# Kernel tuning notes

Hardware: AMD Instinct MI355X
Metric: run time of the kernel (lower is better)

Reference implementation:

```python
import jax, jax.numpy as jnp
import numpy as np
from jax import lax

VOCAB, EMB, H, L_CTX = 5, 64, 256, 100
HG = 2 * H  # generator hidden = 512


def lstm_cell(x, h, c, Wih, Whh, b):
    # PyTorch gate order: i, f, g, o
    z = x @ Wih.T + h @ Whh.T + b
    i, f, g, o = jnp.split(z, 4, axis=-1)
    c = jax.nn.sigmoid(f) * c + jax.nn.sigmoid(i) * jnp.tanh(g)
    h = jax.nn.sigmoid(o) * jnp.tanh(c)
    return h, c


def run_lstm(xs, Wih, Whh, b, hidden):
    # xs: [T, B, D] -> ys: [T, B, hidden]
    B = xs.shape[1]
    h0 = jnp.zeros((B, hidden), xs.dtype)

    def step(carry, x):
        h, c = carry
        h, c = lstm_cell(x, h, c, Wih, Whh, b)
        return (h, c), h

    _, ys = lax.scan(step, (h0, h0), xs)
    return ys


def bidir_layer(xs, Wih, Whh, b):
    # Wih/Whh/b stacked over directions: [2, ...]
    yf = run_lstm(xs, Wih[0], Whh[0], b[0], H)
    yb = run_lstm(xs[::-1], Wih[1], Whh[1], b[1], H)[::-1]
    return jnp.concatenate([yf, yb], axis=-1)  # [T, B, 2H]


def setup_inputs() -> dict:
    key = jax.random.key(0)
    ks = iter(jax.random.split(key, 24))
    s = 1.0 / np.sqrt(H)  # pytorch-style uniform scale -> use normal*s

    def w(shape):
        return (jax.random.normal(next(ks), shape, jnp.float32) * s).astype(jnp.float32)

    B = 1024
    inp = {
        "left_context": jax.random.randint(next(ks), (B, L_CTX), 0, VOCAB),
        "right_context": jax.random.randint(next(ks), (B, L_CTX), 0, VOCAB),
        "target_length": 256,
        "emb": w((VOCAB, EMB)),
        # bidirectional context LSTM, layer 0 (in=64) and layer 1 (in=512)
        "ctx0_Wih": w((2, 4 * H, EMB)),
        "ctx0_Whh": w((2, 4 * H, H)),
        "ctx0_b": w((2, 4 * H)),
        "ctx1_Wih": w((2, 4 * H, 2 * H)),
        "ctx1_Whh": w((2, 4 * H, H)),
        "ctx1_b": w((2, 4 * H)),
        # generator LSTM (hidden=512), layer 0 (in=64) and layer 1 (in=512)
        "gen0_Wih": w((4 * HG, EMB)),
        "gen0_Whh": w((4 * HG, HG)),
        "gen0_b": w((4 * HG,)),
        "gen1_Wih": w((4 * HG, HG)),
        "gen1_Whh": w((4 * HG, HG)),
        "gen1_b": w((4 * HG,)),
        "out_W": w((VOCAB, HG)),
        "out_b": w((VOCAB,)),
    }
    return inp


def reference(left_context, right_context, target_length, emb,
              ctx0_Wih, ctx0_Whh, ctx0_b, ctx1_Wih, ctx1_Whh, ctx1_b,
              gen0_Wih, gen0_Whh, gen0_b, gen1_Wih, gen1_Whh, gen1_b,
              out_W, out_b):
    B = left_context.shape[0]

    def encode(tokens):
        x = emb[tokens].transpose(1, 0, 2)          # [L, B, 64]
        x = bidir_layer(x, ctx0_Wih, ctx0_Whh, ctx0_b)  # dropout: eval -> identity
        x = bidir_layer(x, ctx1_Wih, ctx1_Whh, ctx1_b)
        return x                                     # [L, B, 512]

    left_final = encode(left_context)[-1]            # [B, 512]
    right_final = encode(right_context)[0]           # [B, 512]
    combined = (left_final + right_final) * 0.5

    # h_0 = combined repeated over both generator layers; c_0 = 0
    zeros = jnp.zeros((B, HG), combined.dtype)
    tok0 = jnp.zeros((B,), jnp.int32)

    def dec_step(carry, _):
        h0, c0, h1, c1, tok = carry
        x = emb[tok]                                 # [B, 64]
        h0, c0 = lstm_cell(x, h0, c0, gen0_Wih, gen0_Whh, gen0_b)
        h1, c1 = lstm_cell(h0, h1, c1, gen1_Wih, gen1_Whh, gen1_b)
        logits = h1 @ out_W.T + out_b                # dropout: eval -> identity
        tok = jnp.argmax(logits, axis=-1)
        return (h0, c0, h1, c1, tok), logits

    _, logits = lax.scan(dec_step, (combined, zeros, combined, zeros, tok0),
                         None, length=target_length)
    return logits.transpose(1, 0, 2)                 # [B, T, vocab]
```

## Files before the change

### kernel.cpp

```cpp
#include <hip/hip_runtime.h>


#define L_SEQ 100
#define BATCH 1024
#define HCTX 256
#define HG 512
#define TDEC 256

typedef __attribute__((ext_vector_type(8))) short bf16x8;
typedef __attribute__((ext_vector_type(4))) float f32x4;

__device__ __forceinline__ float sigf(float x){ return 1.0f/(1.0f+expf(-x)); }
__device__ __forceinline__ unsigned short f2bf(float x){
  unsigned int u = __float_as_uint(x);
  return (unsigned short)((u + 0x7fffu + ((u>>16)&1u)) >> 16);
}
__device__ __forceinline__ float bf2f(unsigned short h){
  return __uint_as_float(((unsigned int)h)<<16);
}

__global__ void pack_w(const float* __restrict__ W, int G, int K, int KTtot, int kt0,
                       unsigned short* __restrict__ hi, unsigned short* __restrict__ lo){
  int idx = blockIdx.x*blockDim.x + threadIdx.x;
  int kt_n = K/32;
  int total = (G/16)*kt_n*64;
  if (idx >= total) return;
  int lane = idx & 63;
  int ktl = (idx>>6) % kt_n;
  int gt  = (idx>>6) / kt_n;
  int g = gt*16 + (lane & 15);
  int k = ktl*32 + (lane>>4)*8;
  const float* src = W + (size_t)g*K + k;
  size_t dst = (((size_t)gt*KTtot + (kt0 + ktl))*64 + lane)*8;
  #pragma unroll
  for (int j=0;j<8;j++){
    float x = src[j];
    unsigned short h = f2bf(x);
    hi[dst+j] = h;
    lo[dst+j] = f2bf(x - bf2f(h));
  }
}

__global__ void embprep(const float* __restrict__ emb,
                        const float* __restrict__ c0Wih, const float* __restrict__ c0b,
                        const float* __restrict__ g0Wih, const float* __restrict__ g0b,
                        float* __restrict__ ectx0, float* __restrict__ egen0){
  int idx = blockIdx.x*blockDim.x + threadIdx.x;
  if (idx < 2*5*1024){
    int d = idx / 5120;
    int v = (idx / 1024) % 5;
    int j = idx % 1024;
    const float* w = c0Wih + ((size_t)d*1024 + j)*64;
    const float* e = emb + v*64;
    float s = c0b[d*1024 + j];
    #pragma unroll
    for (int k=0;k<64;k++) s += e[k]*w[k];
    ectx0[idx] = s;
  } else if (idx < 2*5*1024 + 5*2048){
    int i2 = idx - 10240;
    int v = i2 / 2048;
    int j = i2 % 2048;
    const float* w = g0Wih + (size_t)j*64;
    const float* e = emb + v*64;
    float s = g0b[j];
    #pragma unroll
    for (int k=0;k<64;k++) s += e[k]*w[k];
    egen0[i2] = s;
  }
}

__global__ void __launch_bounds__(512,1) ctx_l0_mfma(
    const int* __restrict__ toks,
    const float* __restrict__ ectx0,
    const unsigned short* __restrict__ wh, const unsigned short* __restrict__ wl,
    unsigned short* __restrict__ y0h, unsigned short* __restrict__ y0l)
{
  const int id  = blockIdx.x;
  const int dir = (id >> 2) & 1;
  const int bx  = ((id >> 3) << 2) | (id & 3);
  const int e0  = bx * 16;
  const int lane = threadIdx.x & 63;
  const int w    = threadIdx.x >> 6;
  const int lo16 = lane & 15, kgrp = lane >> 4;

  __shared__ unsigned short hsh[16*256];
  __shared__ unsigned short hsl[16*256];
  __shared__ float cs[16*256];
  for (int i=threadIdx.x;i<16*256;i+=512){ hsh[i]=0; hsl[i]=0; cs[i]=0.f; }
  __syncthreads();

  const unsigned short* pbh[4][2];
  const unsigned short* pbl[4][2];
  #pragma unroll
  for (int g=0;g<4;g++){
    #pragma unroll
    for (int st=0;st<2;st++){
      int ct = g*16 + w*2 + st;
      size_t off = (size_t)dir*1024*256 + ((size_t)(ct*8)*64 + lane)*8;
      pbh[g][st] = wh + off; pbl[g][st] = wl + off;
    }
  }
  const unsigned aoff0 = (unsigned)(lo16*512 + kgrp*16);
  const unsigned axor  = ((unsigned)(lo16 & 7)) << 4;

  for (int s=0;s<L_SEQ;s++){
    const int t = dir ? (L_SEQ-1-s) : s;
    f32x4 zero = {0.f,0.f,0.f,0.f};
    f32x4 acc[4][2];
    #pragma unroll
    for (int g=0;g<4;g++){
      #pragma unroll
      for (int st=0;st<2;st++) acc[g][st] = zero;
    }
    #pragma unroll 2
    for (int kt=0;kt<8;kt++){
      unsigned ao = (aoff0 + kt*64) ^ axor;
      bf16x8 ah = *(const bf16x8*)((const char*)hsh + ao);
      bf16x8 al = *(const bf16x8*)((const char*)hsl + ao);
      #pragma unroll
      for (int g=0;g<4;g++){
        #pragma unroll
        for (int st=0;st<2;st++){
          bf16x8 bh = *(const bf16x8*)(pbh[g][st] + (size_t)kt*512);
          bf16x8 bl = *(const bf16x8*)(pbl[g][st] + (size_t)kt*512);
          acc[g][st] = __builtin_amdgcn_mfma_f32_16x16x32_bf16(ah,bh,acc[g][st],0,0,0);
          acc[g][st] = __builtin_amdgcn_mfma_f32_16x16x32_bf16(al,bh,acc[g][st],0,0,0);
          acc[g][st] = __builtin_amdgcn_mfma_f32_16x16x32_bf16(ah,bl,acc[g][st],0,0,0);
        }
      }
    }
    __syncthreads();
    int tkr[4];
    #pragma unroll
    for (int r=0;r<4;r++) tkr[r] = toks[(e0 + kgrp*4 + r)*L_SEQ + t];
    #pragma unroll
    for (int st=0;st<2;st++){
      const int unit = w*32 + st*16 + lo16;
      #pragma unroll
      for (int r=0;r<4;r++){
        const int row = kgrp*4 + r;
        const int e = e0 + row;
        const float* ep = ectx0 + ((size_t)(dir*5 + tkr[r]))*1024 + unit;
        float zi = acc[0][st][r] + ep[0];
        float zf = acc[1][st][r] + ep[256];
        float zg = acc[2][st][r] + ep[512];
        float zo = acc[3][st][r] + ep[768];
        int ci = row*256 + unit;
        float c = sigf(zf)*cs[ci] + sigf(zi)*tanhf(zg);
        float h = sigf(zo)*tanhf(c);
        cs[ci] = c;
        unsigned short hb = f2bf(h), lb = f2bf(h - bf2f(hb));
        unsigned hoff = ((unsigned)(row*512 + unit*2)) ^ (((unsigned)(row & 7)) << 4);
        *(unsigned short*)((char*)hsh + hoff) = hb;
        *(unsigned short*)((char*)hsl + hoff) = lb;
        size_t yo = ((size_t)t*BATCH + e)*512 + dir*256 + unit;
        y0h[yo] = hb; y0l[yo] = lb;
      }
    }
    __syncthreads();
  }
}

__global__ void __launch_bounds__(512,1) ctx_l1_mfma(
    const unsigned short* __restrict__ y0h, const unsigned short* __restrict__ y0l,
    const unsigned short* __restrict__ wh, const unsigned short* __restrict__ wl,
    const float* __restrict__ bias,
    float* __restrict__ finals, int t_store)
{
  const int id  = blockIdx.x;
  const int dir = (id >> 2) & 1;
  const int bx  = ((id >> 3) << 2) | (id & 3);
  const int e0  = bx * 16;
  const int lane = threadIdx.x & 63;
  const int w    = threadIdx.x >> 6;
  const int lo16 = lane & 15, kgrp = lane >> 4;

  __shared__ unsigned short xsh[16*512];
  __shared__ unsigned short xsl[16*512];
  __shared__ unsigned short hsh[16*256];
  __shared__ unsigned short hsl[16*256];
  __shared__ float cs[16*256];
  for (int i=threadIdx.x;i<16*256;i+=512){ hsh[i]=0; hsl[i]=0; cs[i]=0.f; }

  float bb[4][2];
  #pragma unroll
  for (int g=0;g<4;g++){
    #pragma unroll
    for (int st=0;st<2;st++)
      bb[g][st] = bias[dir*1024 + g*256 + w*32 + st*16 + lo16];
  }
  const unsigned short* pbh[4][2];
  const unsigned short* pbl[4][2];
  #pragma unroll
  for (int g=0;g<4;g++){
    #pragma unroll
    for (int st=0;st<2;st++){
      int ct = g*16 + w*2 + st;
      size_t off = (size_t)dir*1024*768 + ((size_t)(ct*24)*64 + lane)*8;
      pbh[g][st] = wh + off; pbl[g][st] = wl + off;
    }
  }
  const unsigned axor = ((unsigned)(lo16 & 7)) << 4;
  __syncthreads();

  for (int s=0;s<L_SEQ;s++){
    const int t = dir ? (L_SEQ-1-s) : s;
    #pragma unroll
    for (int cc=0; cc<2; cc++){
      int ci = threadIdx.x + cc*512;
      int row = ci >> 6, cr = ci & 63;
      const unsigned short* srcbase = y0h + ((size_t)t*BATCH + e0 + row)*512 + cr*8;
      const unsigned short* srcbasel = y0l + ((size_t)t*BATCH + e0 + row)*512 + cr*8;
      uint4 vh = *(const uint4*)srcbase;
      uint4 vl = *(const uint4*)srcbasel;
      unsigned xo = ((unsigned)(row*1024 + cr*16)) ^ (((unsigned)(row & 7)) << 4);
      *(uint4*)((char*)xsh + xo) = vh;
      *(uint4*)((char*)xsl + xo) = vl;
    }
    __syncthreads();
    f32x4 zero = {0.f,0.f,0.f,0.f};
    f32x4 acc[4][2];
    #pragma unroll
    for (int g=0;g<4;g++){
      #pragma unroll
      for (int st=0;st<2;st++) acc[g][st] = zero;
    }
    #pragma unroll 2
    for (int kt=0;kt<16;kt++){
      unsigned ao = ((unsigned)(lo16*1024 + kt*64 + kgrp*16)) ^ axor;
      bf16x8 ah = *(const bf16x8*)((const char*)xsh + ao);
      bf16x8 al = *(const bf16x8*)((const char*)xsl + ao);
      #pragma unroll
      for (int g=0;g<4;g++){
        #pragma unroll
        for (int st=0;st<2;st++){
          bf16x8 bh = *(const bf16x8*)(pbh[g][st] + (size_t)kt*512);
          bf16x8 bl = *(const bf16x8*)(pbl[g][st] + (size_t)kt*512);
          acc[g][st] = __builtin_amdgcn_mfma_f32_16x16x32_bf16(ah,bh,acc[g][st],0,0,0);
          acc[g][st] = __builtin_amdgcn_mfma_f32_16x16x32_bf16(al,bh,acc[g][st],0,0,0);
          acc[g][st] = __builtin_amdgcn_mfma_f32_16x16x32_bf16(ah,bl,acc[g][st],0,0,0);
        }
      }
    }
    #pragma unroll 2
    for (int kt=16;kt<24;kt++){
      unsigned ao = ((unsigned)(lo16*512 + (kt-16)*64 + kgrp*16)) ^ axor;
      bf16x8 ah = *(const bf16x8*)((const char*)hsh + ao);
      bf16x8 al = *(const bf16x8*)((const char*)hsl + ao);
      #pragma unroll
      for (int g=0;g<4;g++){
        #pragma unroll
        for (int st=0;st<2;st++){
          bf16x8 bh = *(const bf16x8*)(pbh[g][st] + (size_t)kt*512);
          bf16x8 bl = *(const bf16x8*)(pbl[g][st] + (size_t)kt*512);
          acc[g][st] = __builtin_amdgcn_mfma_f32_16x16x32_bf16(ah,bh,acc[g][st],0,0,0);
          acc[g][st] = __builtin_amdgcn_mfma_f32_16x16x32_bf16(al,bh,acc[g][st],0,0,0);
          acc[g][st] = __builtin_amdgcn_mfma_f32_16x16x32_bf16(ah,bl,acc[g][st],0,0,0);
        }
      }
    }
    __syncthreads();
    #pragma unroll
    for (int st=0;st<2;st++){
      const int unit = w*32 + st*16 + lo16;
      #pragma unroll
      for (int r=0;r<4;r++){
        const int row = kgrp*4 + r;
        float zi = acc[0][st][r] + bb[0][st];
        float zf = acc[1][st][r] + bb[1][st];
        float zg = acc[2][st][r] + bb[2][st];
        float zo = acc[3][st][r] + bb[3][st];
        int ci = row*256 + unit;
        float c = sigf(zf)*cs[ci] + sigf(zi)*tanhf(zg);
        float h = sigf(zo)*tanhf(c);
        cs[ci] = c;
        unsigned short hb = f2bf(h), lb = f2bf(h - bf2f(hb));
        unsigned hoff = ((unsigned)(row*512 + unit*2)) ^ (((unsigned)(row & 7)) << 4);
        *(unsigned short*)((char*)hsh + hoff) = hb;
        *(unsigned short*)((char*)hsl + hoff) = lb;
        if (t == t_store)
          finals[(size_t)(e0 + row)*512 + dir*256 + unit] = h;
      }
    }
    __syncthreads();
  }
}

__global__ void combine_init2(const float* __restrict__ lf, const float* __restrict__ rf,
                              unsigned short* __restrict__ h0h, unsigned short* __restrict__ h0l,
                              unsigned short* __restrict__ h1h, unsigned short* __restrict__ h1l,
                              float* __restrict__ c0, float* __restrict__ c1){
  int i = blockIdx.x*blockDim.x + threadIdx.x;
  if (i < BATCH*HG){
    float v = 0.5f*(lf[i]+rf[i]);
    unsigned short h = f2bf(v);
    unsigned short l = f2bf(v - bf2f(h));
    h0h[i]=h; h0l[i]=l; h1h[i]=h; h1l[i]=l;
    c0[i]=0.f; c1[i]=0.f;
  }
}

__global__ void __launch_bounds__(512,1) dec_l0_mfma(
    const float* __restrict__ egen0,
    const unsigned short* __restrict__ wh, const unsigned short* __restrict__ wl,
    const unsigned short* __restrict__ hih, const unsigned short* __restrict__ hil,
    const unsigned short* __restrict__ h1ih, const unsigned short* __restrict__ h1il,
    unsigned short* __restrict__ hoh, unsigned short* __restrict__ hol,
    float* __restrict__ cst,
    const float* __restrict__ outW, const float* __restrict__ outb,
    float* __restrict__ out, int t)
{
  __shared__ unsigned short bsm[2][32768];
  const int bid = blockIdx.x;
  const int by = bid & 15;
  const int bx = bid >> 4;
  const int e0 = bx * 64;
  const int lane = threadIdx.x & 63;
  const int w = threadIdx.x >> 6;
  const int wm = w & 3, wu = w >> 2;
  const int ut = by*2 + wu;
  const int lo16 = lane & 15, kgrp = lane >> 4;
  const int arow = e0 + wm*16 + lo16;
  const int u = ut*16 + lo16;
  const int r0 = e0 + wm*16 + kgrp*4;

  const unsigned short* pah = hih + (size_t)arow*512 + kgrp*8;
  const unsigned short* pal = hil + (size_t)arow*512 + kgrp*8;

  auto STAGE = [&](int c){
    #pragma unroll
    for (int i=0;i<8;i++){
      int id = w*8 + i;
      int hl  = id & 1;
      int q   = (id >> 1) & 3;
      int wu2 = (id >> 3) & 1;
      int ksl = id >> 4;
      int ks  = c*4 + ksl;
      const unsigned short* src = (hl ? wl : wh)
          + (((size_t)(q*32 + by*2 + wu2)*16 + ks)*64 + lane)*8;
      __builtin_amdgcn_global_load_lds((const void*)src,
          (void*)(&bsm[c & 1][id*512]), 16, 0, 0);
    }
  };

  const f32x4 z4 = {0.f,0.f,0.f,0.f};
  f32x4 aHH[4]={z4,z4,z4,z4}, aLH[4]={z4,z4,z4,z4}, aHL[4]={z4,z4,z4,z4};

  STAGE(0);
  __syncthreads();
  for (int c=0; c<4; c++){
    if (c+1 < 4) STAGE(c+1);
    const unsigned short* bb = &bsm[c&1][0];
    #pragma unroll
    for (int ksl=0; ksl<4; ksl++){
      int ks = c*4 + ksl;
      bf16x8 ah = *(const bf16x8*)(pah + (size_t)ks*32);
      bf16x8 al = *(const bf16x8*)(pal + (size_t)ks*32);
      #pragma unroll
      for (int q=0;q<4;q++){
        int fid = ((ksl*2 + wu)*4 + q)*2;
        bf16x8 bh = *(const bf16x8*)(bb + fid*512     + lane*8);
        bf16x8 bl = *(const bf16x8*)(bb + fid*512+512 + lane*8);
        aHH[q] = __builtin_amdgcn_mfma_f32_16x16x32_bf16(ah, bh, aHH[q], 0,0,0);
        aLH[q] = __builtin_amdgcn_mfma_f32_16x16x32_bf16(al, bh, aLH[q], 0,0,0);
        aHL[q] = __builtin_amdgcn_mfma_f32_16x16x32_bf16(ah, bl, aHL[q], 0,0,0);
      }
    }
    __syncthreads();
  }

  int tkr[4] = {0,0,0,0};
  if (t > 0){
    float acc5[4][5];
    #pragma unroll
    for (int r=0;r<4;r++){
      #pragma unroll
      for (int v=0;v<5;v++) acc5[r][v]=0.f;
    }
    #pragma unroll
    for (int j=0;j<4;j++){
      const int ub = lo16*32 + j*8;
      f32x4 w0[5], w1[5];
      #pragma unroll
      for (int v=0;v<5;v++){
        const float* wp = outW + v*512 + ub;
        w0[v] = *(const f32x4*)(wp);
        w1[v] = *(const f32x4*)(wp+4);
      }
      #pragma unroll
      for (int r=0;r<4;r++){
        const unsigned short* hh = h1ih + (size_t)(r0+r)*512 + ub;
        const unsigned short* hl = h1il + (size_t)(r0+r)*512 + ub;
        bf16x8 vh = *(const bf16x8*)hh;
        bf16x8 vl = *(const bf16x8*)hl;
        #pragma unroll
        for (int m=0;m<4;m++){
          float hv = bf2f((unsigned short)vh[m]) + bf2f((unsigned short)vl[m]);
          #pragma unroll
          for (int v=0;v<5;v++) acc5[r][v] += hv * w0[v][m];
        }
        #pragma unroll
        for (int m=0;m<4;m++){
          float hv = bf2f((unsigned short)vh[m+4]) + bf2f((unsigned short)vl[m+4]);
          #pragma unroll
          for (int v=0;v<5;v++) acc5[r][v] += hv * w1[v][m];
        }
      }
    }
    #pragma unroll
    for (int r=0;r<4;r++){
      #pragma unroll
      for (int v=0;v<5;v++){
        float s = acc5[r][v];
        s += __shfl_xor(s, 1);
        s += __shfl_xor(s, 2);
        s += __shfl_xor(s, 4);
        s += __shfl_xor(s, 8);
        acc5[r][v] = s + outb[v];
      }
      float best = acc5[r][0]; int tk = 0;
      if (acc5[r][1] > best){ best = acc5[r][1]; tk = 1; }
      if (acc5[r][2] > best){ best = acc5[r][2]; tk = 2; }
      if (acc5[r][3] > best){ best = acc5[r][3]; tk = 3; }
      if (acc5[r][4] > best){ best = acc5[r][4]; tk = 4; }
      tkr[r] = tk;
    }
    if (by == 0 && wu == 0 && lo16 == 0){
      #pragma unroll
      for (int r=0;r<4;r++){
        float* op = out + ((size_t)(r0+r)*TDEC + (t-1))*5;
        #pragma unroll
        for (int v=0;v<5;v++) op[v] = acc5[r][v];
      }
    }
  }

  #pragma unroll
  for (int r=0;r<4;r++){
    const int e = r0 + r;
    const float* ep = egen0 + (size_t)tkr[r]*2048 + u;
    float zi = aHH[0][r]+aLH[0][r]+aHL[0][r] + ep[0];
    float zf = aHH[1][r]+aLH[1][r]+aHL[1][r] + ep[512];
    float zg = aHH[2][r]+aLH[2][r]+aHL[2][r] + ep[1024];
    float zo = aHH[3][r]+aLH[3][r]+aHL[3][r] + ep[1536];
    const size_t idx = (size_t)e*512 + u;
    float c = sigf(zf)*cst[idx] + sigf(zi)*tanhf(zg);
    float h = sigf(zo)*tanhf(c);
    cst[idx] = c;
    unsigned short hb = f2bf(h);
    hoh[idx] = hb;
    hol[idx] = f2bf(h - bf2f(hb));
  }
}

__global__ void __launch_bounds__(512,1) dec_l1_mfma(
    const unsigned short* __restrict__ xh, const unsigned short* __restrict__ xl,
    const unsigned short* __restrict__ wh, const unsigned short* __restrict__ wl,
    const float* __restrict__ bias,
    const unsigned short* __restrict__ hih, const unsigned short* __restrict__ hil,
    unsigned short* __restrict__ hoh, unsigned short* __restrict__ hol,
    float* __restrict__ cst)
{
  __shared__ unsigned short bsm[2][32768];
  const int bid = blockIdx.x;
  const int by = bid & 15;
  const int bx = bid >> 4;
  const int e0 = bx * 64;
  const int lane = threadIdx.x & 63;
  const int w = threadIdx.x >> 6;
  const int wm = w & 3, wu = w >> 2;
  const int ut = by*2 + wu;
  const int lo16 = lane & 15, kgrp = lane >> 4;
  const int arow = e0 + wm*16 + lo16;
  const int u = ut*16 + lo16;
  const int r0 = e0 + wm*16 + kgrp*4;

  const unsigned short* pxh = xh  + (size_t)arow*512 + kgrp*8;
  const unsigned short* pxl = xl  + (size_t)arow*512 + kgrp*8;
  const unsigned short* pah = hih + (size_t)arow*512 + kgrp*8;
  const unsigned short* pal = hil + (size_t)arow*512 + kgrp*8;

  auto STAGE = [&](int c){
    #pragma unroll
    for (int i=0;i<8;i++){
      int id = w*8 + i;
      int hl  = id & 1;
      int q   = (id >> 1) & 3;
      int wu2 = (id >> 3) & 1;
      int ksl = id >> 4;
      int ks  = c*4 + ksl;
      const unsigned short* src = (hl ? wl : wh)
          + (((size_t)(q*32 + by*2 + wu2)*32 + ks)*64 + lane)*8;
      __builtin_amdgcn_global_load_lds((const void*)src,
          (void*)(&bsm[c & 1][id*512]), 16, 0, 0);
    }
  };

  const f32x4 z4 = {0.f,0.f,0.f,0.f};
  f32x4 aHH[4]={z4,z4,z4,z4}, aLH[4]={z4,z4,z4,z4}, aHL[4]={z4,z4,z4,z4};

  STAGE(0);
  __syncthreads();
  for (int c=0; c<8; c++){
    if (c+1 < 8) STAGE(c+1);
    const unsigned short* bb = &bsm[c&1][0];
    const unsigned short* pAh = (c < 4) ? pxh : pah;
    const unsigned short* pAl = (c < 4) ? pxl : pal;
    const int ksA = (c & 3)*4;
    #pragma unroll
    for (int ksl=0; ksl<4; ksl++){
      bf16x8 ah = *(const bf16x8*)(pAh + (size_t)(ksA+ksl)*32);
      bf16x8 al = *(const bf16x8*)(pAl + (size_t)(ksA+ksl)*32);
      #pragma unroll
      for (int q=0;q<4;q++){
        int fid = ((ksl*2 + wu)*4 + q)*2;
        bf16x8 bh = *(const bf16x8*)(bb + fid*512     + lane*8);
        bf16x8 bl = *(const bf16x8*)(bb + fid*512+512 + lane*8);
        aHH[q] = __builtin_amdgcn_mfma_f32_16x16x32_bf16(ah, bh, aHH[q], 0,0,0);
        aLH[q] = __builtin_amdgcn_mfma_f32_16x16x32_bf16(al, bh, aLH[q], 0,0,0);
        aHL[q] = __builtin_amdgcn_mfma_f32_16x16x32_bf16(ah, bl, aHL[q], 0,0,0);
      }
    }
    __syncthreads();
  }

  const float b0 = bias[u], b1 = bias[512+u], b2 = bias[1024+u], b3 = bias[1536+u];
  #pragma unroll
  for (int r=0;r<4;r++){
    const int e = r0 + r;
    float zi = aHH[0][r]+aLH[0][r]+aHL[0][r] + b0;
    float zf = aHH[1][r]+aLH[1][r]+aHL[1][r] + b1;
    float zg = aHH[2][r]+aLH[2][r]+aHL[2][r] + b2;
    float zo = aHH[3][r]+aLH[3][r]+aHL[3][r] + b3;
    const size_t idx = (size_t)e*512 + u;
    float c = sigf(zf)*cst[idx] + sigf(zi)*tanhf(zg);
    float h = sigf(zo)*tanhf(c);
    cst[idx] = c;
    unsigned short hb = f2bf(h);
    hoh[idx] = hb;
    hol[idx] = f2bf(h - bf2f(hb));
  }
}

__global__ void dec_outF(const unsigned short* __restrict__ h1h,
                         const unsigned short* __restrict__ h1l,
                         const float* __restrict__ outW,
                         const float* __restrict__ outb,
                         float* __restrict__ out){
  const int lane = threadIdx.x & 63;
  const int e = blockIdx.x*4 + (threadIdx.x >> 6);
  const unsigned short* hh = h1h + (size_t)e*512;
  const unsigned short* hl = h1l + (size_t)e*512;
  float s0=0,s1=0,s2=0,s3=0,s4=0;
  for (int k=lane;k<512;k+=64){
    float hv = bf2f(hh[k]) + bf2f(hl[k]);
    s0 += hv*outW[k];
    s1 += hv*outW[512+k];
    s2 += hv*outW[1024+k];
    s3 += hv*outW[1536+k];
    s4 += hv*outW[2048+k];
  }
  #pragma unroll
  for (int off=32; off>0; off>>=1){
    s0 += __shfl_down(s0, off);
    s1 += __shfl_down(s1, off);
    s2 += __shfl_down(s2, off);
    s3 += __shfl_down(s3, off);
    s4 += __shfl_down(s4, off);
  }
  if (lane==0){
    float* op = out + ((size_t)e*TDEC + (TDEC-1))*5;
    op[0]=s0+outb[0]; op[1]=s1+outb[1]; op[2]=s2+outb[2];
    op[3]=s3+outb[3]; op[4]=s4+outb[4];
  }
}

extern "C" void kernel_launch(void* const* d_in, const int* in_sizes, int n_in,
                              void* d_out, int out_size, void* d_ws, size_t ws_size,
                              hipStream_t stream){
  (void)in_sizes; (void)n_in; (void)out_size;
  const int*   leftc    = (const int*)d_in[0];
  const int*   rightc   = (const int*)d_in[1];
  const float* emb      = (const float*)d_in[3];
  const float* ctx0_Wih = (const float*)d_in[4];
  const float* ctx0_Whh = (const float*)d_in[5];
  const float* ctx0_b   = (const float*)d_in[6];
  const float* ctx1_Wih = (const float*)d_in[7];
  const float* ctx1_Whh = (const float*)d_in[8];
  const float* ctx1_b   = (const float*)d_in[9];
  const float* gen0_Wih = (const float*)d_in[10];
  const float* gen0_Whh = (const float*)d_in[11];
  const float* gen0_b   = (const float*)d_in[12];
  const float* gen1_Wih = (const float*)d_in[13];
  const float* gen1_Whh = (const float*)d_in[14];
  const float* gen1_b   = (const float*)d_in[15];
  const float* out_W    = (const float*)d_in[16];
  const float* out_b    = (const float*)d_in[17];
  float* out = (float*)d_out;

  char* p = (char*)d_ws;
  auto carve = [&](size_t nfloats)->float*{
    float* r = (float*)p;
    p += ((nfloats*sizeof(float) + 255) & ~(size_t)255);
    return r;
  };
  auto carveu = [&](size_t nush)->unsigned short*{
    return (unsigned short*)carve((nush + 1)/2);
  };
  float* ectx0  = carve(2*5*1024);
  float* egen0  = carve(5*2048);
  float* leftF  = carve((size_t)BATCH*HG);
  float* rightF = carve((size_t)BATCH*HG);
  float* c0s    = carve((size_t)BATCH*HG);
  float* c1s    = carve((size_t)BATCH*HG);
  unsigned short* c0pkh = carveu((size_t)2*1024*256);
  unsigned short* c0pkl = carveu((size_t)2*1024*256);
  unsigned short* c1pkh = carveu((size_t)2*1024*768);
  unsigned short* c1pkl = carveu((size_t)2*1024*768);
  unsigned short* pk0h = carveu((size_t)2048*512);
  unsigned short* pk0l = carveu((size_t)2048*512);
  unsigned short* pk1h = carveu((size_t)2048*1024);
  unsigned short* pk1l = carveu((size_t)2048*1024);
  unsigned short* h0ha = carveu((size_t)BATCH*HG);
  unsigned short* h0la = carveu((size_t)BATCH*HG);
  unsigned short* h0hb = carveu((size_t)BATCH*HG);
  unsigned short* h0lb = carveu((size_t)BATCH*HG);
  unsigned short* h1ha = carveu((size_t)BATCH*HG);
  unsigned short* h1la = carveu((size_t)BATCH*HG);
  unsigned short* h1hb = carveu((size_t)BATCH*HG);
  unsigned short* h1lb = carveu((size_t)BATCH*HG);
  unsigned short* y0h = carveu((size_t)L_SEQ*BATCH*512);
  unsigned short* y0l = carveu((size_t)L_SEQ*BATCH*512);
  if ((size_t)(p - (char*)d_ws) > ws_size) return;

  for (int d=0; d<2; d++){
    pack_w<<<128, 256, 0, stream>>>(ctx0_Whh + (size_t)d*1024*256, 1024, 256, 8, 0,
                                    c0pkh + (size_t)d*262144, c0pkl + (size_t)d*262144);
    pack_w<<<256, 256, 0, stream>>>(ctx1_Wih + (size_t)d*1024*512, 1024, 512, 24, 0,
                                    c1pkh + (size_t)d*786432, c1pkl + (size_t)d*786432);
    pack_w<<<128, 256, 0, stream>>>(ctx1_Whh + (size_t)d*1024*256, 1024, 256, 24, 16,
                                    c1pkh + (size_t)d*786432, c1pkl + (size_t)d*786432);
  }
  pack_w<<<512, 256, 0, stream>>>(gen0_Whh, 2048, 512, 16,  0, pk0h, pk0l);
  pack_w<<<512, 256, 0, stream>>>(gen1_Wih, 2048, 512, 32,  0, pk1h, pk1l);
  pack_w<<<512, 256, 0, stream>>>(gen1_Whh, 2048, 512, 32, 16, pk1h, pk1l);

  embprep<<<(20480+255)/256, 256, 0, stream>>>(emb, ctx0_Wih, ctx0_b,
                                               gen0_Wih, gen0_b, ectx0, egen0);

  ctx_l0_mfma<<<128, 512, 0, stream>>>(leftc, ectx0, c0pkh, c0pkl, y0h, y0l);
  ctx_l1_mfma<<<128, 512, 0, stream>>>(y0h, y0l, c1pkh, c1pkl, ctx1_b, leftF, L_SEQ-1);
  ctx_l0_mfma<<<128, 512, 0, stream>>>(rightc, ectx0, c0pkh, c0pkl, y0h, y0l);
  ctx_l1_mfma<<<128, 512, 0, stream>>>(y0h, y0l, c1pkh, c1pkl, ctx1_b, rightF, 0);

  combine_init2<<<(BATCH*HG+255)/256, 256, 0, stream>>>(leftF, rightF,
                                                        h0ha, h0la, h1ha, h1la,
                                                        c0s, c1s);

  for (int t=0;t<TDEC;t++){
    unsigned short* h0ih = (t&1)? h0hb : h0ha;
    unsigned short* h0il = (t&1)? h0lb : h0la;
    unsigned short* h0oh = (t&1)? h0ha : h0hb;
    unsigned short* h0ol = (t&1)? h0la : h0lb;
    unsigned short* h1ih = (t&1)? h1hb : h1ha;
    unsigned short* h1il = (t&1)? h1lb : h1la;
    unsigned short* h1oh = (t&1)? h1ha : h1hb;
    unsigned short* h1ol = (t&1)? h1la : h1lb;
    dec_l0_mfma<<<256, 512, 0, stream>>>(egen0, pk0h, pk0l,
                                         h0ih, h0il, h1ih, h1il,
                                         h0oh, h0ol, c0s,
                                         out_W, out_b, out, t);
    dec_l1_mfma<<<256, 512, 0, stream>>>(h0oh, h0ol, pk1h, pk1l, gen1_b,
                                         h1ih, h1il, h1oh, h1ol, c1s);
  }
  dec_outF<<<256, 256, 0, stream>>>(h1ha, h1la, out_W, out_b, out);
}
```

Baseline: 22.96 ms.

## Fuse decoder time loop into one persistent cooperative kernel with grid sync

Replaces the 512 per-step decoder kernel launches with a single cooperative kernel that loops over all 256 timesteps and uses grid.sync between layers. LSTM cell states now stay in registers instead of global memory, and the first weight stage of the next layer is prefetched across phase boundaries. This is meant to remove launch overhead and cell-state traffic. The cost is two grid-wide barriers per step, and it requires all 256 blocks to be co-resident.

After: 44.38 ms. 93.3% more time.

```diff
diff --git a/kernel.cpp b/kernel.cpp
--- a/kernel.cpp
+++ b/kernel.cpp
@@ -1,4 +1,7 @@
 #include <hip/hip_runtime.h>
+#include <hip/hip_cooperative_groups.h>
+
+namespace cg = cooperative_groups;
 
 
 #define L_SEQ 100
@@ -288,28 +291,29 @@
 
 __global__ void combine_init2(const float* __restrict__ lf, const float* __restrict__ rf,
                               unsigned short* __restrict__ h0h, unsigned short* __restrict__ h0l,
-                              unsigned short* __restrict__ h1h, unsigned short* __restrict__ h1l,
-                              float* __restrict__ c0, float* __restrict__ c1){
+                              unsigned short* __restrict__ h1h, unsigned short* __restrict__ h1l){
   int i = blockIdx.x*blockDim.x + threadIdx.x;
   if (i < BATCH*HG){
     float v = 0.5f*(lf[i]+rf[i]);
     unsigned short h = f2bf(v);
     unsigned short l = f2bf(v - bf2f(h));
     h0h[i]=h; h0l[i]=l; h1h[i]=h; h1l[i]=l;
-    c0[i]=0.f; c1[i]=0.f;
-  }
-}
-
-__global__ void __launch_bounds__(512,1) dec_l0_mfma(
+  }
+}
+
+__global__ void __launch_bounds__(512,1) dec_persist(
     const float* __restrict__ egen0,
-    const unsigned short* __restrict__ wh, const unsigned short* __restrict__ wl,
-    const unsigned short* __restrict__ hih, const unsigned short* __restrict__ hil,
-    const unsigned short* __restrict__ h1ih, const unsigned short* __restrict__ h1il,
-    unsigned short* __restrict__ hoh, unsigned short* __restrict__ hol,
-    float* __restrict__ cst,
+    const unsigned short* __restrict__ w0h, const unsigned short* __restrict__ w0l,
+    const unsigned short* __restrict__ w1h, const unsigned short* __restrict__ w1l,
+    const float* __restrict__ bias1,
     const float* __restrict__ outW, const float* __restrict__ outb,
-    float* __restrict__ out, int t)
+    unsigned short* __restrict__ h0ha, unsigned short* __restrict__ h0la,
+    unsigned short* __restrict__ h0hb, unsigned short* __restrict__ h0lb,
+    unsigned short* __restrict__ h1ha, unsigned short* __restrict__ h1la,
+    unsigned short* __restrict__ h1hb, unsigned short* __restrict__ h1lb,
+    float* __restrict__ out)
 {
+  cg::grid_group grid = cg::this_grid();
   __shared__ unsigned short bsm[2][32768];
   const int bid = blockIdx.x;
   const int by = bid & 15;
@@ -324,10 +328,10 @@
   const int u = ut*16 + lo16;
   const int r0 = e0 + wm*16 + kgrp*4;
 
-  const unsigned short* pah = hih + (size_t)arow*512 + kgrp*8;
-  const unsigned short* pal = hil + (size_t)arow*512 + kgrp*8;
-
-  auto STAGE = [&](int c){
+  const float b10 = bias1[u], b11 = bias1[512+u];
+  const float b12 = bias1[1024+u], b13 = bias1[1536+u];
+
+  auto STAGE0 = [&](int c){
     #pragma unroll
     for (int i=0;i<8;i++){
       int id = w*8 + i;
@@ -336,151 +340,13 @@
       int wu2 = (id >> 3) & 1;
       int ksl = id >> 4;
       int ks  = c*4 + ksl;
-      const unsigned short* src = (hl ? wl : wh)
+      const unsigned short* src = (hl ? w0l : w0h)
           + (((size_t)(q*32 + by*2 + wu2)*16 + ks)*64 + lane)*8;
       __builtin_amdgcn_global_load_lds((const void*)src,
           (void*)(&bsm[c & 1][id*512]), 16, 0, 0);
     }
   };
-
-  const f32x4 z4 = {0.f,0.f,0.f,0.f};
-  f32x4 aHH[4]={z4,z4,z4,z4}, aLH[4]={z4,z4,z4,z4}, aHL[4]={z4,z4,z4,z4};
-
-  STAGE(0);
-  __syncthreads();
-  for (int c=0; c<4; c++){
-    if (c+1 < 4) STAGE(c+1);
-    const unsigned short* bb = &bsm[c&1][0];
-    #pragma unroll
-    for (int ksl=0; ksl<4; ksl++){
-      int ks = c*4 + ksl;
-      bf16x8 ah = *(const bf16x8*)(pah + (size_t)ks*32);
-      bf16x8 al = *(const bf16x8*)(pal + (size_t)ks*32);
-      #pragma unroll
-      for (int q=0;q<4;q++){
-        int fid = ((ksl*2 + wu)*4 + q)*2;
-        bf16x8 bh = *(const bf16x8*)(bb + fid*512     + lane*8);
-        bf16x8 bl = *(const bf16x8*)(bb + fid*512+512 + lane*8);
-        aHH[q] = __builtin_amdgcn_mfma_f32_16x16x32_bf16(ah, bh, aHH[q], 0,0,0);
-        aLH[q] = __builtin_amdgcn_mfma_f32_16x16x32_bf16(al, bh, aLH[q], 0,0,0);
-        aHL[q] = __builtin_amdgcn_mfma_f32_16x16x32_bf16(ah, bl, aHL[q], 0,0,0);
-      }
-    }
-    __syncthreads();
-  }
-
-  int tkr[4] = {0,0,0,0};
-  if (t > 0){
-    float acc5[4][5];
-    #pragma unroll
-    for (int r=0;r<4;r++){
-      #pragma unroll
-      for (int v=0;v<5;v++) acc5[r][v]=0.f;
-    }
-    #pragma unroll
-    for (int j=0;j<4;j++){
-      const int ub = lo16*32 + j*8;
-      f32x4 w0[5], w1[5];
-      #pragma unroll
-      for (int v=0;v<5;v++){
-        const float* wp = outW + v*512 + ub;
-        w0[v] = *(const f32x4*)(wp);
-        w1[v] = *(const f32x4*)(wp+4);
-      }
-      #pragma unroll
-      for (int r=0;r<4;r++){
-        const unsigned short* hh = h1ih + (size_t)(r0+r)*512 + ub;
-        const unsigned short* hl = h1il + (size_t)(r0+r)*512 + ub;
-        bf16x8 vh = *(const bf16x8*)hh;
-        bf16x8 vl = *(const bf16x8*)hl;
-        #pragma unroll
-        for (int m=0;m<4;m++){
-          float hv = bf2f((unsigned short)vh[m]) + bf2f((unsigned short)vl[m]);
-          #pragma unroll
-          for (int v=0;v<5;v++) acc5[r][v] += hv * w0[v][m];
-        }
-        #pragma unroll
-        for (int m=0;m<4;m++){
-          float hv = bf2f((unsigned short)vh[m+4]) + bf2f((unsigned short)vl[m+4]);
-          #pragma unroll
-          for (int v=0;v<5;v++) acc5[r][v] += hv * w1[v][m];
-        }
-      }
-    }
-    #pragma unroll
-    for (int r=0;r<4;r++){
-      #pragma unroll
-      for (int v=0;v<5;v++){
-        float s = acc5[r][v];
-        s += __shfl_xor(s, 1);
-        s += __shfl_xor(s, 2);
-        s += __shfl_xor(s, 4);
-        s += __shfl_xor(s, 8);
-        acc5[r][v] = s + outb[v];
-      }
-      float best = acc5[r][0]; int tk = 0;
-      if (acc5[r][1] > best){ best = acc5[r][1]; tk = 1; }
-      if (acc5[r][2] > best){ best = acc5[r][2]; tk = 2; }
-      if (acc5[r][3] > best){ best = acc5[r][3]; tk = 3; }
-      if (acc5[r][4] > best){ best = acc5[r][4]; tk = 4; }
-      tkr[r] = tk;
-    }
-    if (by == 0 && wu == 0 && lo16 == 0){
-      #pragma unroll
-      for (int r=0;r<4;r++){
-        float* op = out + ((size_t)(r0+r)*TDEC + (t-1))*5;
-        #pragma unroll
-        for (int v=0;v<5;v++) op[v] = acc5[r][v];
-      }
-    }
-  }
-
-  #pragma unroll
-  for (int r=0;r<4;r++){
-    const int e = r0 + r;
-    const float* ep = egen0 + (size_t)tkr[r]*2048 + u;
-    float zi = aHH[0][r]+aLH[0][r]+aHL[0][r] + ep[0];
-    float zf = aHH[1][r]+aLH[1][r]+aHL[1][r] + ep[512];
-    float zg = aHH[2][r]+aLH[2][r]+aHL[2][r] + ep[1024];
-    float zo = aHH[3][r]+aLH[3][r]+aHL[3][r] + ep[1536];
-    const size_t idx = (size_t)e*512 + u;
-    float c = sigf(zf)*cst[idx] + sigf(zi)*tanhf(zg);
-    float h = sigf(zo)*tanhf(c);
-    cst[idx] = c;
-    unsigned short hb = f2bf(h);
-    hoh[idx] = hb;
-    hol[idx] = f2bf(h - bf2f(hb));
-  }
-}
-
-__global__ void __launch_bounds__(512,1) dec_l1_mfma(
-    const unsigned short* __restrict__ xh, const unsigned short* __restrict__ xl,
-    const unsigned short* __restrict__ wh, const unsigned short* __restrict__ wl,
-    const float* __restrict__ bias,
-    const unsigned short* __restrict__ hih, const unsigned short* __restrict__ hil,
-    unsigned short* __restrict__ hoh, unsigned short* __restrict__ hol,
-    float* __restrict__ cst)
-{
-  __shared__ unsigned short bsm[2][32768];
-  const int bid = blockIdx.x;
-  const int by = bid & 15;
-  const int bx = bid >> 4;
-  const int e0 = bx * 64;
-  const int lane = threadIdx.x & 63;
-  const int w = threadIdx.x >> 6;
-  const int wm = w & 3, wu = w >> 2;
-  const int ut = by*2 + wu;
-  const int lo16 = lane & 15, kgrp = lane >> 4;
-  const int arow = e0 + wm*16 + lo16;
-  const int u = ut*16 + lo16;
-  const int r0 = e0 + wm*16 + kgrp*4;
-
-  const unsigned short* pxh = xh  + (size_t)arow*512 + kgrp*8;
-  const unsigned short* pxl = xl  + (size_t)arow*512 + kgrp*8;
-  const unsigned short* pah = hih + (size_t)arow*512 + kgrp*8;
-  const unsigned short* pal = hil + (size_t)arow*512 + kgrp*8;
-
-  auto STAGE = [&](int c){
+  auto STAGE1 = [&](int c){
     #pragma unroll
     for (int i=0;i<8;i++){
       int id = w*8 + i;
@@ -489,56 +355,186 @@
       int wu2 = (id >> 3) & 1;
       int ksl = id >> 4;
       int ks  = c*4 + ksl;
-      const unsigned short* src = (hl ? wl : wh)
+      const unsigned short* src = (hl ? w1l : w1h)
           + (((size_t)(q*32 + by*2 + wu2)*32 + ks)*64 + lane)*8;
       __builtin_amdgcn_global_load_lds((const void*)src,
           (void*)(&bsm[c & 1][id*512]), 16, 0, 0);
     }
   };
 
+  float c0r[4] = {0.f,0.f,0.f,0.f};
+  float c1r[4] = {0.f,0.f,0.f,0.f};
   const f32x4 z4 = {0.f,0.f,0.f,0.f};
-  f32x4 aHH[4]={z4,z4,z4,z4}, aLH[4]={z4,z4,z4,z4}, aHL[4]={z4,z4,z4,z4};
-
-  STAGE(0);
-  __syncthreads();
-  for (int c=0; c<8; c++){
-    if (c+1 < 8) STAGE(c+1);
-    const unsigned short* bb = &bsm[c&1][0];
-    const unsigned short* pAh = (c < 4) ? pxh : pah;
-    const unsigned short* pAl = (c < 4) ? pxl : pal;
-    const int ksA = (c & 3)*4;
-    #pragma unroll
-    for (int ksl=0; ksl<4; ksl++){
-      bf16x8 ah = *(const bf16x8*)(pAh + (size_t)(ksA+ksl)*32);
-      bf16x8 al = *(const bf16x8*)(pAl + (size_t)(ksA+ksl)*32);
-      #pragma unroll
-      for (int q=0;q<4;q++){
-        int fid = ((ksl*2 + wu)*4 + q)*2;
-        bf16x8 bh = *(const bf16x8*)(bb + fid*512     + lane*8);
-        bf16x8 bl = *(const bf16x8*)(bb + fid*512+512 + lane*8);
-        aHH[q] = __builtin_amdgcn_mfma_f32_16x16x32_bf16(ah, bh, aHH[q], 0,0,0);
-        aLH[q] = __builtin_amdgcn_mfma_f32_16x16x32_bf16(al, bh, aLH[q], 0,0,0);
-        aHL[q] = __builtin_amdgcn_mfma_f32_16x16x32_bf16(ah, bl, aHL[q], 0,0,0);
-      }
-    }
-    __syncthreads();
-  }
-
-  const float b0 = bias[u], b1 = bias[512+u], b2 = bias[1024+u], b3 = bias[1536+u];
-  #pragma unroll
-  for (int r=0;r<4;r++){
-    const int e = r0 + r;
-    float zi = aHH[0][r]+aLH[0][r]+aHL[0][r] + b0;
-    float zf = aHH[1][r]+aLH[1][r]+aHL[1][r] + b1;
-    float zg = aHH[2][r]+aLH[2][r]+aHL[2][r] + b2;
-    float zo = aHH[3][r]+aLH[3][r]+aHL[3][r] + b3;
-    const size_t idx = (size_t)e*512 + u;
-    float c = sigf(zf)*cst[idx] + sigf(zi)*tanhf(zg);
-    float h = sigf(zo)*tanhf(c);
-    cst[idx] = c;
-    unsigned short hb = f2bf(h);
-    hoh[idx] = hb;
-    hol[idx] = f2bf(h - bf2f(hb));
+
+  STAGE0(0);
+  for (int t=0;t<TDEC;t++){
+    const unsigned short* h0ih = (t&1)? h0hb : h0ha;
+    const unsigned short* h0il = (t&1)? h0lb : h0la;
+    unsigned short* h0oh = (t&1)? h0ha : h0hb;
+    unsigned short* h0ol = (t&1)? h0la : h0lb;
+    const unsigned short* h1ih = (t&1)? h1hb : h1ha;
+    const unsigned short* h1il = (t&1)? h1lb : h1la;
+    unsigned short* h1oh = (t&1)? h1ha : h1hb;
+    unsigned short* h1ol = (t&1)? h1la : h1lb;
+
+    {
+      __syncthreads();
+      const unsigned short* pah = h0ih + (size_t)arow*512 + kgrp*8;
+      const unsigned short* pal = h0il + (size_t)arow*512 + kgrp*8;
+      f32x4 aHH[4]={z4,z4,z4,z4}, aLH[4]={z4,z4,z4,z4}, aHL[4]={z4,z4,z4,z4};
+      for (int c=0; c<4; c++){
+        if (c < 3) STAGE0(c+1); else STAGE1(0);
+        const unsigned short* bb = &bsm[c&1][0];
+        #pragma unroll
+        for (int ksl=0; ksl<4; ksl++){
+          int ks = c*4 + ksl;
+          bf16x8 ah = *(const bf16x8*)(pah + (size_t)ks*32);
+          bf16x8 al = *(const bf16x8*)(pal + (size_t)ks*32);
+          #pragma unroll
+          for (int q=0;q<4;q++){
+            int fid = ((ksl*2 + wu)*4 + q)*2;
+            bf16x8 bh = *(const bf16x8*)(bb + fid*512     + lane*8);
+            bf16x8 bl = *(const bf16x8*)(bb + fid*512+512 + lane*8);
+            aHH[q] = __builtin_amdgcn_mfma_f32_16x16x32_bf16(ah, bh, aHH[q], 0,0,0);
+            aLH[q] = __builtin_amdgcn_mfma_f32_16x16x32_bf16(al, bh, aLH[q], 0,0,0);
+            aHL[q] = __builtin_amdgcn_mfma_f32_16x16x32_bf16(ah, bl, aHL[q], 0,0,0);
+          }
+        }
+        __syncthreads();
+      }
+
+      int tkr[4] = {0,0,0,0};
+      if (t > 0){
+        float acc5[4][5];
+        #pragma unroll
+        for (int r=0;r<4;r++){
+          #pragma unroll
+          for (int v=0;v<5;v++) acc5[r][v]=0.f;
+        }
+        #pragma unroll
+        for (int j=0;j<4;j++){
+          const int ub = lo16*32 + j*8;
+          f32x4 w0[5], w1[5];
+          #pragma unroll
+          for (int v=0;v<5;v++){
+            const float* wp = outW + v*512 + ub;
+            w0[v] = *(const f32x4*)(wp);
+            w1[v] = *(const f32x4*)(wp+4);
+          }
+          #pragma unroll
+          for (int r=0;r<4;r++){
+            const unsigned short* hh = h1ih + (size_t)(r0+r)*512 + ub;
+            const unsigned short* hl = h1il + (size_t)(r0+r)*512 + ub;
+            bf16x8 vh = *(const bf16x8*)hh;
+            bf16x8 vl = *(const bf16x8*)hl;
+            #pragma unroll
+            for (int m=0;m<4;m++){
+              float hv = bf2f((unsigned short)vh[m]) + bf2f((unsigned short)vl[m]);
+              #pragma unroll
+              for (int v=0;v<5;v++) acc5[r][v] += hv * w0[v][m];
+            }
+            #pragma unroll
+            for (int m=0;m<4;m++){
+              float hv = bf2f((unsigned short)vh[m+4]) + bf2f((unsigned short)vl[m+4]);
+              #pragma unroll
+              for (int v=0;v<5;v++) acc5[r][v] += hv * w1[v][m];
+            }
+          }
+        }
+        #pragma unroll
+        for (int r=0;r<4;r++){
+          #pragma unroll
+          for (int v=0;v<5;v++){
+            float s = acc5[r][v];
+            s += __shfl_xor(s, 1);
+            s += __shfl_xor(s, 2);
+            s += __shfl_xor(s, 4);
+            s += __shfl_xor(s, 8);
+            acc5[r][v] = s + outb[v];
+          }
+          float best = acc5[r][0]; int tk = 0;
+          if (acc5[r][1] > best){ best = acc5[r][1]; tk = 1; }
+          if (acc5[r][2] > best){ best = acc5[r][2]; tk = 2; }
+          if (acc5[r][3] > best){ best = acc5[r][3]; tk = 3; }
+          if (acc5[r][4] > best){ best = acc5[r][4]; tk = 4; }
+          tkr[r] = tk;
+        }
+        if (by == 0 && wu == 0 && lo16 == 0){
+          #pragma unroll
+          for (int r=0;r<4;r++){
+            float* op = out + ((size_t)(r0+r)*TDEC + (t-1))*5;
+            #pragma unroll
+            for (int v=0;v<5;v++) op[v] = acc5[r][v];
+          }
+        }
+      }
+
+      #pragma unroll
+      for (int r=0;r<4;r++){
+        const int e = r0 + r;
+        const float* ep = egen0 + (size_t)tkr[r]*2048 + u;
+        float zi = aHH[0][r]+aLH[0][r]+aHL[0][r] + ep[0];
+        float zf = aHH[1][r]+aLH[1][r]+aHL[1][r] + ep[512];
+        float zg = aHH[2][r]+aLH[2][r]+aHL[2][r] + ep[1024];
+        float zo = aHH[3][r]+aLH[3][r]+aHL[3][r] + ep[1536];
+        float c = sigf(zf)*c0r[r] + sigf(zi)*tanhf(zg);
+        float h = sigf(zo)*tanhf(c);
+        c0r[r] = c;
+        const size_t idx = (size_t)e*512 + u;
+        unsigned short hb = f2bf(h);
+        h0oh[idx] = hb;
+        h0ol[idx] = f2bf(h - bf2f(hb));
+      }
+    }
+    grid.sync();
+
+    {
+      const unsigned short* pxh = h0oh + (size_t)arow*512 + kgrp*8;
+      const unsigned short* pxl = h0ol + (size_t)arow*512 + kgrp*8;
+      const unsigned short* pah = h1ih + (size_t)arow*512 + kgrp*8;
+      const unsigned short* pal = h1il + (size_t)arow*512 + kgrp*8;
+      f32x4 aHH[4]={z4,z4,z4,z4}, aLH[4]={z4,z4,z4,z4}, aHL[4]={z4,z4,z4,z4};
+      for (int c=0; c<8; c++){
+        if (c < 7) STAGE1(c+1);
+        else if (t+1 < TDEC) STAGE0(0);
+        const unsigned short* bb = &bsm[c&1][0];
+        const unsigned short* pAh = (c < 4) ? pxh : pah;
+        const unsigned short* pAl = (c < 4) ? pxl : pal;
+        const int ksA = (c & 3)*4;
+        #pragma unroll
+        for (int ksl=0; ksl<4; ksl++){
+          bf16x8 ah = *(const bf16x8*)(pAh + (size_t)(ksA+ksl)*32);
+          bf16x8 al = *(const bf16x8*)(pAl + (size_t)(ksA+ksl)*32);
+          #pragma unroll
+          for (int q=0;q<4;q++){
+            int fid = ((ksl*2 + wu)*4 + q)*2;
+            bf16x8 bh = *(const bf16x8*)(bb + fid*512     + lane*8);
+            bf16x8 bl = *(const bf16x8*)(bb + fid*512+512 + lane*8);
+            aHH[q] = __builtin_amdgcn_mfma_f32_16x16x32_bf16(ah, bh, aHH[q], 0,0,0);
+            aLH[q] = __builtin_amdgcn_mfma_f32_16x16x32_bf16(al, bh, aLH[q], 0,0,0);
+            aHL[q] = __builtin_amdgcn_mfma_f32_16x16x32_bf16(ah, bl, aHL[q], 0,0,0);
+          }
+        }
+        __syncthreads();
+      }
+
+      #pragma unroll
+      for (int r=0;r<4;r++){
+        const int e = r0 + r;
+        float zi = aHH[0][r]+aLH[0][r]+aHL[0][r] + b10;
+        float zf = aHH[1][r]+aLH[1][r]+aHL[1][r] + b11;
+        float zg = aHH[2][r]+aLH[2][r]+aHL[2][r] + b12;
+        float zo = aHH[3][r]+aLH[3][r]+aHL[3][r] + b13;
+        float c = sigf(zf)*c1r[r] + sigf(zi)*tanhf(zg);
+        float h = sigf(zo)*tanhf(c);
+        c1r[r] = c;
+        const size_t idx = (size_t)e*512 + u;
+        unsigned short hb = f2bf(h);
+        h1oh[idx] = hb;
+        h1ol[idx] = f2bf(h - bf2f(hb));
+      }
+    }
+    grid.sync();
   }
 }
 
@@ -611,8 +607,6 @@
   float* egen0  = carve(5*2048);
   float* leftF  = carve((size_t)BATCH*HG);
   float* rightF = carve((size_t)BATCH*HG);
-  float* c0s    = carve((size_t)BATCH*HG);
-  float* c1s    = carve((size_t)BATCH*HG);
   unsigned short* c0pkh = carveu((size_t)2*1024*256);
   unsigned short* c0pkl = carveu((size_t)2*1024*256);
   unsigned short* c1pkh = carveu((size_t)2*1024*768);
@@ -654,24 +648,17 @@
   ctx_l1_mfma<<<128, 512, 0, stream>>>(y0h, y0l, c1pkh, c1pkl, ctx1_b, rightF, 0);
 
   combine_init2<<<(BATCH*HG+255)/256, 256, 0, stream>>>(leftF, rightF,
-                                                        h0ha, h0la, h1ha, h1la,
-                                                        c0s, c1s);
-
-  for (int t=0;t<TDEC;t++){
-    unsigned short* h0ih = (t&1)? h0hb : h0ha;
-    unsigned short* h0il = (t&1)? h0lb : h0la;
-    unsigned short* h0oh = (t&1)? h0ha : h0hb;
-    unsigned short* h0ol = (t&1)? h0la : h0lb;
-    unsigned short* h1ih = (t&1)? h1hb : h1ha;
-    unsigned short* h1il = (t&1)? h1lb : h1la;
-    unsigned short* h1oh = (t&1)? h1ha : h1hb;
-    unsigned short* h1ol = (t&1)? h1la : h1lb;
-    dec_l0_mfma<<<256, 512, 0, stream>>>(egen0, pk0h, pk0l,
-                                         h0ih, h0il, h1ih, h1il,
-                                         h0oh, h0ol, c0s,
-                                         out_W, out_b, out, t);
-    dec_l1_mfma<<<256, 512, 0, stream>>>(h0oh, h0ol, pk1h, pk1l, gen1_b,
-                                         h1ih, h1il, h1oh, h1ol, c1s);
-  }
+                                                        h0ha, h0la, h1ha, h1la);
+
+  void* kargs[] = {
+    (void*)&egen0, (void*)&pk0h, (void*)&pk0l, (void*)&pk1h, (void*)&pk1l,
+    (void*)&gen1_b, (void*)&out_W, (void*)&out_b,
+    (void*)&h0ha, (void*)&h0la, (void*)&h0hb, (void*)&h0lb,
+    (void*)&h1ha, (void*)&h1la, (void*)&h1hb, (void*)&h1lb,
+    (void*)&out
+  };
+  hipLaunchCooperativeKernel((void*)dec_persist, dim3(256), dim3(512),
+                             kargs, 0, stream);
+
   dec_outF<<<256, 256, 0, stream>>>(h1ha, h1la, out_W, out_b, out);
 }
```
